# Kernel tuning notes

Measured on AMD Instinct MI355X. Metric: run time of the kernel, lower is better.

## Reference

```python
import jax, jax.numpy as jnp
import numpy as np

B, L, D = 1, 4096, 1024
N_AR, N_DIFF, D_HEAD = 8, 8, 64
H = N_AR + N_DIFF
ROPE_BASE = 10000.0


def rotate_half(x):
    x1, x2 = jnp.split(x, 2, axis=-1)
    return jnp.concatenate([-x2, x1], axis=-1)


def rope_cos_sin(seq_len, d_head):
    inv_freq = 1.0 / (ROPE_BASE ** (jnp.arange(0, d_head, 2, dtype=jnp.float32) / d_head))
    t = jnp.arange(seq_len, dtype=jnp.float32)
    freqs = t[:, None] * inv_freq[None, :]          # [L, d_head//2]
    emb = jnp.concatenate([freqs, freqs], axis=-1)  # [L, d_head]
    return jnp.cos(emb), jnp.sin(emb)


def setup_inputs() -> dict:
    key = jax.random.key(0)
    ks = jax.random.split(key, 5)
    return {
        "hidden_states": jax.random.normal(ks[0], (B, L, D), dtype=jnp.float32),
        "Wq": jax.random.normal(ks[1], (D, H * D_HEAD), dtype=jnp.float32) * 0.02,
        "Wk": jax.random.normal(ks[2], (D, H * D_HEAD), dtype=jnp.float32) * 0.02,
        "Wv": jax.random.normal(ks[3], (D, H * D_HEAD), dtype=jnp.float32) * 0.02,
        "Wo": jax.random.normal(ks[4], (H * D_HEAD, D), dtype=jnp.float32) * 0.02,
    }


def _attend(q, k, v, mask):
    # q,k,v: [B, h, L, d]; mask: [L, L] additive
    scale = D_HEAD ** -0.5
    scores = jnp.einsum("bhqd,bhkd->bhqk", q, k) * scale + mask
    attn = jax.nn.softmax(scores.astype(jnp.float32), axis=-1).astype(q.dtype)
    return jnp.einsum("bhqk,bhkd->bhqd", attn, v)


def reference(hidden_states, Wq, Wk, Wv, Wo):
    b, l, _ = hidden_states.shape

    def heads(x, W):
        return (x @ W).reshape(b, l, H, D_HEAD).transpose(0, 2, 1, 3)  # [B,H,L,d]

    q = heads(hidden_states, Wq)
    k = heads(hidden_states, Wk)
    v = heads(hidden_states, Wv)

    cos, sin = rope_cos_sin(l, D_HEAD)  # [L, d]
    q = q * cos + rotate_half(q) * sin
    k = k * cos + rotate_half(k) * sin

    neg_inf = jnp.finfo(jnp.float32).min
    causal = jnp.where(jnp.tril(jnp.ones((l, l), dtype=bool)), 0.0, -jnp.inf).astype(jnp.float32)

    out_ar = _attend(q[:, :N_AR], k[:, :N_AR], v[:, :N_AR], causal)
    out_diff = _attend(q[:, N_AR:], k[:, N_AR:], v[:, N_AR:], jnp.zeros((l, l), jnp.float32))

    out = jnp.concatenate([out_ar, out_diff], axis=1)          # [B,H,L,d]
    out = out.transpose(0, 2, 1, 3).reshape(b, l, H * D_HEAD)  # [B,L,H*d]
    return out @ Wo
```

## Files before the change

kernel.cpp:

```cpp
#include <hip/hip_runtime.h>

#define LSEQ 4096
#define DMODEL 1024
#define HTOT 16
#define NAR 8
#define DHEAD 64
#define QKVS 3072

typedef unsigned short u16;
typedef unsigned int u32;
typedef __attribute__((ext_vector_type(8))) short bf16x8;
typedef __attribute__((ext_vector_type(4))) short bf16x4;
typedef __attribute__((ext_vector_type(4))) float f32x4;
typedef __attribute__((ext_vector_type(4))) unsigned int u32x4;

typedef __attribute__((address_space(1))) void gvoid;
typedef __attribute__((address_space(3))) void lvoid;

__device__ __forceinline__ void cp16(const void* g, void* l) {
    __builtin_amdgcn_global_load_lds((gvoid*)(void*)g, (lvoid*)l, 16, 0, 0);
}

__device__ __forceinline__ float bfs(u16 v) { return __uint_as_float((u32)v << 16); }
__device__ __forceinline__ u16 f2bf(float f) {
    u32 x = __float_as_uint(f);
    return (u16)((x + 0x7fffu + ((x >> 16) & 1u)) >> 16);
}
__device__ __forceinline__ u32 pack2(float a, float b) {
    return (u32)f2bf(a) | ((u32)f2bf(b) << 16);
}
__device__ __forceinline__ u32 packtr(float lo, float hi) {
    return __builtin_amdgcn_perm(__float_as_uint(hi), __float_as_uint(lo), 0x07060302u);
}

__global__ __launch_bounds__(256) void transp_cvt3(
    const float* __restrict__ Wq, const float* __restrict__ Wk,
    const float* __restrict__ Wv, u16* __restrict__ D)
{
    __shared__ u16 T[64][72];
    const float* S = (blockIdx.z == 0) ? Wq : ((blockIdx.z == 1) ? Wk : Wv);
    u16* Dz = D + (size_t)blockIdx.z * 1024 * 1024;
    const int tid = threadIdx.x;
    const int bx = blockIdx.x, by = blockIdx.y;
#pragma unroll
    for (int i = 0; i < 4; ++i) {
        int id = tid + i * 256;
        int fr = id >> 4, fc = id & 15;
        float4 v = *(const float4*)(S + (size_t)(by * 64 + fr) * 1024 + bx * 64 + fc * 4);
        T[fc * 4 + 0][fr] = f2bf(v.x);
        T[fc * 4 + 1][fr] = f2bf(v.y);
        T[fc * 4 + 2][fr] = f2bf(v.z);
        T[fc * 4 + 3][fr] = f2bf(v.w);
    }
    __syncthreads();
#pragma unroll
    for (int i = 0; i < 2; ++i) {
        int id = tid + i * 256;
        int c = id >> 3, g = id & 7;
        *(uint4*)(Dz + (size_t)(bx * 64 + c) * 1024 + by * 64 + g * 8) = *(const uint4*)&T[c][g * 8];
    }
}

__global__ __launch_bounds__(256) void transp_cvt(
    const float* __restrict__ S, u16* __restrict__ D)
{
    __shared__ u16 T[64][72];
    const int tid = threadIdx.x;
    const int bx = blockIdx.x, by = blockIdx.y;
#pragma unroll
    for (int i = 0; i < 4; ++i) {
        int id = tid + i * 256;
        int fr = id >> 4, fc = id & 15;
        float4 v = *(const float4*)(S + (size_t)(by * 64 + fr) * 1024 + bx * 64 + fc * 4);
        T[fc * 4 + 0][fr] = f2bf(v.x);
        T[fc * 4 + 1][fr] = f2bf(v.y);
        T[fc * 4 + 2][fr] = f2bf(v.z);
        T[fc * 4 + 3][fr] = f2bf(v.w);
    }
    __syncthreads();
#pragma unroll
    for (int i = 0; i < 2; ++i) {
        int id = tid + i * 256;
        int c = id >> 3, g = id & 7;
        *(uint4*)(D + (size_t)(bx * 64 + c) * 1024 + by * 64 + g * 8) = *(const uint4*)&T[c][g * 8];
    }
}

__global__ __launch_bounds__(256) void gemm_qkv(
    const float* __restrict__ A, const u16* __restrict__ Bt, u16* __restrict__ C)
{
    __shared__ u16 As[2][128][40];
    __shared__ u16 Bs[2][128][32];
    const int tid = threadIdx.x;
    const int lane = tid & 63, w = tid >> 6;
    const int col = lane & 15, quad = lane >> 4;
    const int bm = blockIdx.y << 7, bn = blockIdx.x << 7;
    const int wm = (w & 1) << 6, wn = (w >> 1) << 6;
    const int sr = lane >> 2, sc = (lane & 3) << 3;
    const int ar0 = tid >> 2, ag = (tid & 3) << 3;
    const f32x4 zero = {0.f, 0.f, 0.f, 0.f};
    f32x4 acc[4][4];
#pragma unroll
    for (int i = 0; i < 4; ++i)
#pragma unroll
        for (int j = 0; j < 4; ++j) acc[i][j] = zero;

    {
#pragma unroll
        for (int i = 0; i < 2; ++i)
            cp16(Bt + (size_t)(bn + w * 32 + i * 16 + sr) * 1024 + sc, &Bs[0][w * 32 + i * 16][0]);
        float4 a0[2], a1[2];
#pragma unroll
        for (int it = 0; it < 2; ++it) {
            const float* ap = A + (size_t)(bm + ar0 + it * 64) * 1024 + ag;
            a0[it] = *(const float4*)ap;
            a1[it] = *(const float4*)(ap + 4);
        }
#pragma unroll
        for (int it = 0; it < 2; ++it) {
            uint4 pk;
            pk.x = pack2(a0[it].x, a0[it].y); pk.y = pack2(a0[it].z, a0[it].w);
            pk.z = pack2(a1[it].x, a1[it].y); pk.w = pack2(a1[it].z, a1[it].w);
            *(uint4*)&As[0][ar0 + it * 64][ag] = pk;
        }
    }

    for (int kc = 0; kc < 32; ++kc) {
        const int cur = kc & 1, nxt = cur ^ 1;
        __syncthreads();
        const bool pre = (kc + 1 < 32);
        float4 a0[2], a1[2];
        if (pre) {
            const int k1 = (kc + 1) * 32;
#pragma unroll
            for (int i = 0; i < 2; ++i)
                cp16(Bt + (size_t)(bn + w * 32 + i * 16 + sr) * 1024 + k1 + sc,
                     &Bs[nxt][w * 32 + i * 16][0]);
#pragma unroll
            for (int it = 0; it < 2; ++it) {
                const float* ap = A + (size_t)(bm + ar0 + it * 64) * 1024 + k1 + ag;
                a0[it] = *(const float4*)ap;
                a1[it] = *(const float4*)(ap + 4);
            }
        }
        bf16x8 af[4], bfr[4];
#pragma unroll
        for (int i = 0; i < 4; ++i) af[i] = *(const bf16x8*)&As[cur][wm + i * 16 + col][quad * 8];
#pragma unroll
        for (int j = 0; j < 4; ++j) bfr[j] = *(const bf16x8*)&Bs[cur][wn + j * 16 + col][quad * 8];
#pragma unroll
        for (int i = 0; i < 4; ++i)
#pragma unroll
            for (int j = 0; j < 4; ++j)
                acc[i][j] = __builtin_amdgcn_mfma_f32_16x16x32_bf16(af[i], bfr[j], acc[i][j], 0, 0, 0);
        if (pre) {
#pragma unroll
            for (int it = 0; it < 2; ++it) {
                uint4 pk;
                pk.x = pack2(a0[it].x, a0[it].y); pk.y = pack2(a0[it].z, a0[it].w);
                pk.z = pack2(a1[it].x, a1[it].y); pk.w = pack2(a1[it].z, a1[it].w);
                *(uint4*)&As[nxt][ar0 + it * 64][ag] = pk;
            }
        }
    }
#pragma unroll
    for (int i = 0; i < 4; ++i)
#pragma unroll
        for (int j = 0; j < 4; ++j)
#pragma unroll
            for (int r = 0; r < 4; ++r)
                C[(size_t)(bm + wm + i * 16 + quad * 4 + r) * QKVS + bn + wn + j * 16 + col] =
                    f2bf(acc[i][j][r]);
}

__global__ __launch_bounds__(256) void gemm_out(
    const u16* __restrict__ A, const u16* __restrict__ Bt, float* __restrict__ C)
{
    __shared__ u16 As[2][128][32];
    __shared__ u16 Bs[2][128][32];
    const int tid = threadIdx.x;
    const int lane = tid & 63, w = tid >> 6;
    const int col = lane & 15, quad = lane >> 4;
    const int bm = blockIdx.y << 7, bn = blockIdx.x << 7;
    const int wm = (w & 1) << 6, wn = (w >> 1) << 6;
    const int sr = lane >> 2, sc = (lane & 3) << 3;
    const f32x4 zero = {0.f, 0.f, 0.f, 0.f};
    f32x4 acc[4][4];
#pragma unroll
    for (int i = 0; i < 4; ++i)
#pragma unroll
        for (int j = 0; j < 4; ++j) acc[i][j] = zero;

#pragma unroll
    for (int i = 0; i < 2; ++i) {
        const int r0 = w * 32 + i * 16;
        cp16(A  + (size_t)(bm + r0 + sr) * 1024 + sc, &As[0][r0][0]);
        cp16(Bt + (size_t)(bn + r0 + sr) * 1024 + sc, &Bs[0][r0][0]);
    }

    for (int kc = 0; kc < 32; ++kc) {
        const int cur = kc & 1, nxt = cur ^ 1;
        __syncthreads();
        if (kc + 1 < 32) {
            const int k1 = (kc + 1) * 32;
#pragma unroll
            for (int i = 0; i < 2; ++i) {
                const int r0 = w * 32 + i * 16;
                cp16(A  + (size_t)(bm + r0 + sr) * 1024 + k1 + sc, &As[nxt][r0][0]);
                cp16(Bt + (size_t)(bn + r0 + sr) * 1024 + k1 + sc, &Bs[nxt][r0][0]);
            }
        }
        bf16x8 af[4], bfr[4];
#pragma unroll
        for (int i = 0; i < 4; ++i) af[i] = *(const bf16x8*)&As[cur][wm + i * 16 + col][quad * 8];
#pragma unroll
        for (int j = 0; j < 4; ++j) bfr[j] = *(const bf16x8*)&Bs[cur][wn + j * 16 + col][quad * 8];
#pragma unroll
        for (int i = 0; i < 4; ++i)
#pragma unroll
            for (int j = 0; j < 4; ++j)
                acc[i][j] = __builtin_amdgcn_mfma_f32_16x16x32_bf16(af[i], bfr[j], acc[i][j], 0, 0, 0);
    }
#pragma unroll
    for (int i = 0; i < 4; ++i)
#pragma unroll
        for (int j = 0; j < 4; ++j)
#pragma unroll
            for (int r = 0; r < 4; ++r)
                C[(size_t)(bm + wm + i * 16 + quad * 4 + r) * 1024 + bn + wn + j * 16 + col] =
                    acc[i][j][r];
}

__global__ __launch_bounds__(256) void rope_kernel(u16* __restrict__ QKV)
{
    const int idx = blockIdx.x * 256 + threadIdx.x;
    const int i = idx & 31;
    const int h = (idx >> 5) & 15;
    const int t = idx >> 9;
    const float inv = __expf((float)i * -0.2878231366242557f);
    float s, c;
    __sincosf((float)t * inv, &s, &c);
    const size_t base = (size_t)t * QKVS + h * DHEAD + i;
    const float qs = 0.18033688011112042f;

    float q1 = bfs(QKV[base]), q2 = bfs(QKV[base + 32]);
    QKV[base]      = f2bf((q1 * c - q2 * s) * qs);
    QKV[base + 32] = f2bf((q2 * c + q1 * s) * qs);

    const size_t kb = base + 1024;
    float k1 = bfs(QKV[kb]), k2 = bfs(QKV[kb + 32]);
    QKV[kb]      = f2bf(k1 * c - k2 * s);
    QKV[kb + 32] = f2bf(k2 * c + k1 * s);
}

__global__ __launch_bounds__(256) void attn_mfma(
    const u16* __restrict__ QKV, u16* __restrict__ AO)
{
    __shared__ u16 Ks[2][128][64];
    __shared__ u16 Vt[2][64][136];
    const int bid = blockIdx.x;
    int h, qt;
    if (bid < 256) { h = 8 + (bid & 7); qt = bid >> 3; }
    else { int i = bid - 256; h = i & 7; qt = 31 - (i >> 3); }
    const bool causal = (h < NAR);
    const int tid = threadIdx.x;
    const int w = tid >> 6, lane = tid & 63;
    const int col = lane & 15, quad = lane >> 4;
    const int qb = qt * 128;
    const int qr0 = qb + w * 32 + col;
    const int qr1 = qr0 + 16;

    bf16x8 qf[2][2];
#pragma unroll
    for (int s = 0; s < 2; ++s)
#pragma unroll
        for (int ks = 0; ks < 2; ++ks)
            qf[s][ks] = *(const bf16x8*)(QKV + (size_t)(qr0 + s * 16) * QKVS +
                                         h * DHEAD + ks * 32 + quad * 8);

    bf16x4 ones;
    ones[0] = (short)0x3F80; ones[1] = (short)0x3F80;
    ones[2] = (short)0x3F80; ones[3] = (short)0x3F80;

    const f32x4 zero = {0.f, 0.f, 0.f, 0.f};
    f32x4 O[2][5];
#pragma unroll
    for (int s = 0; s < 2; ++s)
#pragma unroll
        for (int nd = 0; nd < 5; ++nd) O[s][nd] = zero;

    const int nch = causal ? (qt + 1) : (LSEQ / 128);
    const int krow = lane >> 3;
    const int kcb = (lane & 7) ^ krow;
    const u16* kbase = QKV + (size_t)krow * QKVS + 1024 + h * DHEAD + kcb * 8;
    const u16* vbase = QKV + (size_t)(lane * 2) * QKVS + 2048 + h * DHEAD + w * 16;

    {
#pragma unroll
        for (int i = 0; i < 4; ++i)
            cp16(kbase + (size_t)((i * 4 + w) * 8) * QKVS, &Ks[0][(i * 4 + w) * 8][0]);
        u32x4 A0 = *(u32x4*)(vbase);
        u32x4 A1 = *(u32x4*)(vbase + 8);
        u32x4 B0 = *(u32x4*)(vbase + QKVS);
        u32x4 B1 = *(u32x4*)(vbase + QKVS + 8);
#pragma unroll
        for (int j = 0; j < 4; ++j) {
            *(u32*)&Vt[0][w * 16 + 2 * j][lane * 2]     = __builtin_amdgcn_perm(B0[j], A0[j], 0x05040100u);
            *(u32*)&Vt[0][w * 16 + 2 * j + 1][lane * 2] = __builtin_amdgcn_perm(B0[j], A0[j], 0x07060302u);
            *(u32*)&Vt[0][w * 16 + 8 + 2 * j][lane * 2]     = __builtin_amdgcn_perm(B1[j], A1[j], 0x05040100u);
            *(u32*)&Vt[0][w * 16 + 8 + 2 * j + 1][lane * 2] = __builtin_amdgcn_perm(B1[j], A1[j], 0x07060302u);
        }
    }

    for (int ch = 0; ch < nch; ++ch) {
        const int cur = ch & 1, nxt = cur ^ 1;
        __syncthreads();
        const bool pre = (ch + 1 < nch);
        u32x4 A0 = {}, A1 = {}, B0 = {}, B1 = {};
        if (pre) {
            const size_t c1 = (size_t)(ch + 1) * 128;
#pragma unroll
            for (int i = 0; i < 4; ++i)
                cp16(kbase + (c1 + (i * 4 + w) * 8) * QKVS, &Ks[nxt][(i * 4 + w) * 8][0]);
            const u16* vp = vbase + c1 * QKVS;
            A0 = *(u32x4*)(vp);
            A1 = *(u32x4*)(vp + 8);
            B0 = *(u32x4*)(vp + QKVS);
            B1 = *(u32x4*)(vp + QKVS + 8);
        }

#pragma unroll
        for (int hf = 0; hf < 2; ++hf) {
            f32x4 st[2][4];
#pragma unroll
            for (int s = 0; s < 2; ++s)
#pragma unroll
                for (int jj = 0; jj < 4; ++jj) st[s][jj] = zero;
#pragma unroll
            for (int jj = 0; jj < 4; ++jj)
#pragma unroll
                for (int ks = 0; ks < 2; ++ks) {
                    bf16x8 kf = *(const bf16x8*)&Ks[cur][(hf * 4 + jj) * 16 + col]
                                                    [((ks * 4 + quad) ^ (col & 7)) * 8];
                    st[0][jj] = __builtin_amdgcn_mfma_f32_16x16x32_bf16(kf, qf[0][ks], st[0][jj], 0, 0, 0);
                    st[1][jj] = __builtin_amdgcn_mfma_f32_16x16x32_bf16(kf, qf[1][ks], st[1][jj], 0, 0, 0);
                }
            if (causal && ch == qt) {
#pragma unroll
                for (int jj = 0; jj < 4; ++jj) {
                    const int kk = ch * 128 + (hf * 4 + jj) * 16 + quad * 4;
#pragma unroll
                    for (int r = 0; r < 4; ++r) {
                        if (kk + r > qr0) st[0][jj][r] = -1e30f;
                        if (kk + r > qr1) st[1][jj][r] = -1e30f;
                    }
                }
            }
            bf16x4 pf[2][4];
#pragma unroll
            for (int s = 0; s < 2; ++s)
#pragma unroll
                for (int jj = 0; jj < 4; ++jj) {
                    u32 lo = packtr(__builtin_amdgcn_exp2f(st[s][jj][0]),
                                    __builtin_amdgcn_exp2f(st[s][jj][1]));
                    u32 hi = packtr(__builtin_amdgcn_exp2f(st[s][jj][2]),
                                    __builtin_amdgcn_exp2f(st[s][jj][3]));
                    u32* p = (u32*)&pf[s][jj];
                    p[0] = lo; p[1] = hi;
                }
#pragma unroll
            for (int nd = 0; nd < 4; ++nd)
#pragma unroll
                for (int jj = 0; jj < 4; ++jj) {
                    bf16x4 vtf = *(const bf16x4*)&Vt[cur][nd * 16 + col][(hf * 4 + jj) * 16 + quad * 4];
                    O[0][nd] = __builtin_amdgcn_mfma_f32_16x16x16bf16_1k(vtf, pf[0][jj], O[0][nd], 0, 0, 0);
                    O[1][nd] = __builtin_amdgcn_mfma_f32_16x16x16bf16_1k(vtf, pf[1][jj], O[1][nd], 0, 0, 0);
                }
#pragma unroll
            for (int jj = 0; jj < 4; ++jj) {
                O[0][4] = __builtin_amdgcn_mfma_f32_16x16x16bf16_1k(ones, pf[0][jj], O[0][4], 0, 0, 0);
                O[1][4] = __builtin_amdgcn_mfma_f32_16x16x16bf16_1k(ones, pf[1][jj], O[1][4], 0, 0, 0);
            }
        }

        if (pre) {
#pragma unroll
            for (int j = 0; j < 4; ++j) {
                *(u32*)&Vt[nxt][w * 16 + 2 * j][lane * 2]     = __builtin_amdgcn_perm(B0[j], A0[j], 0x05040100u);
                *(u32*)&Vt[nxt][w * 16 + 2 * j + 1][lane * 2] = __builtin_amdgcn_perm(B0[j], A0[j], 0x07060302u);
                *(u32*)&Vt[nxt][w * 16 + 8 + 2 * j][lane * 2]     = __builtin_amdgcn_perm(B1[j], A1[j], 0x05040100u);
                *(u32*)&Vt[nxt][w * 16 + 8 + 2 * j + 1][lane * 2] = __builtin_amdgcn_perm(B1[j], A1[j], 0x07060302u);
            }
        }
    }
#pragma unroll
    for (int s = 0; s < 2; ++s) {
        const float inv = 1.f / O[s][4][0];
        const int qrow = qr0 + s * 16;
#pragma unroll
        for (int nd = 0; nd < 4; ++nd) {
            ushort4 ov;
            ov.x = f2bf(O[s][nd][0] * inv);
            ov.y = f2bf(O[s][nd][1] * inv);
            ov.z = f2bf(O[s][nd][2] * inv);
            ov.w = f2bf(O[s][nd][3] * inv);
            *(ushort4*)(AO + (size_t)qrow * 1024 + h * DHEAD + nd * 16 + quad * 4) = ov;
        }
    }
}

extern "C" void kernel_launch(void* const* d_in, const int* in_sizes, int n_in,
                              void* d_out, int out_size, void* d_ws, size_t ws_size,
                              hipStream_t stream)
{
    const float* X  = (const float*)d_in[0];
    const float* Wq = (const float*)d_in[1];
    const float* Wk = (const float*)d_in[2];
    const float* Wv = (const float*)d_in[3];
    const float* Wo = (const float*)d_in[4];
    float* out = (float*)d_out;

    u16* Wt  = (u16*)d_ws;
    u16* AOb = (u16*)d_ws;
    u16* QKV = (u16*)d_ws + (size_t)4 * 1024 * 1024;
    u16* Wot = QKV;

    transp_cvt3<<<dim3(16, 16, 3), 256, 0, stream>>>(Wq, Wk, Wv, Wt);
    gemm_qkv<<<dim3(24, 32), 256, 0, stream>>>(X, Wt, QKV);
    rope_kernel<<<(LSEQ * HTOT * 32) / 256, 256, 0, stream>>>(QKV);
    attn_mfma<<<512, 256, 0, stream>>>(QKV, AOb);
    transp_cvt<<<dim3(16, 16), 256, 0, stream>>>(Wo, Wot);
    gemm_out<<<dim3(8, 32), 256, 0, stream>>>(AOb, Wot, out);
}
```

Baseline: 273.0 us.

## Fuse RoPE into QKV GEMM epilogue and restructure attention to 2-wave software pipeline

RoPE and the Q scaling now run in the QKV GEMM epilogue on fp32 accumulators, so the separate rope kernel and its read-modify-write pass over Q/K are gone. The QKV GEMM also converts its A input to bf16 by truncation (packtr) instead of round-to-nearest, which costs a little accuracy. The attention kernel moves to 128 threads with 64 query rows per wave and a skewed pipeline that overlaps P·V of the previous chunk with QK^T/exp of the current one. This raises per-wave register pressure and halves the threads per block, which may lower occupancy.

```diff
diff --git a/kernel.cpp b/kernel.cpp
--- a/kernel.cpp
+++ b/kernel.cpp
@@ -25,9 +25,6 @@
 __device__ __forceinline__ u16 f2bf(float f) {
     u32 x = __float_as_uint(f);
     return (u16)((x + 0x7fffu + ((x >> 16) & 1u)) >> 16);
-}
-__device__ __forceinline__ u32 pack2(float a, float b) {
-    return (u32)f2bf(a) | ((u32)f2bf(b) << 16);
 }
 __device__ __forceinline__ u32 packtr(float lo, float hi) {
     return __builtin_amdgcn_perm(__float_as_uint(hi), __float_as_uint(lo), 0x07060302u);
@@ -109,18 +106,14 @@
 #pragma unroll
         for (int i = 0; i < 2; ++i)
             cp16(Bt + (size_t)(bn + w * 32 + i * 16 + sr) * 1024 + sc, &Bs[0][w * 32 + i * 16][0]);
-        float4 a0[2], a1[2];
 #pragma unroll
         for (int it = 0; it < 2; ++it) {
             const float* ap = A + (size_t)(bm + ar0 + it * 64) * 1024 + ag;
-            a0[it] = *(const float4*)ap;
-            a1[it] = *(const float4*)(ap + 4);
-        }
-#pragma unroll
-        for (int it = 0; it < 2; ++it) {
+            float4 a0 = *(const float4*)ap;
+            float4 a1 = *(const float4*)(ap + 4);
             uint4 pk;
-            pk.x = pack2(a0[it].x, a0[it].y); pk.y = pack2(a0[it].z, a0[it].w);
-            pk.z = pack2(a1[it].x, a1[it].y); pk.w = pack2(a1[it].z, a1[it].w);
+            pk.x = packtr(a0.x, a0.y); pk.y = packtr(a0.z, a0.w);
+            pk.z = packtr(a1.x, a1.y); pk.w = packtr(a1.z, a1.w);
             *(uint4*)&As[0][ar0 + it * 64][ag] = pk;
         }
     }
@@ -157,11 +150,32 @@
 #pragma unroll
             for (int it = 0; it < 2; ++it) {
                 uint4 pk;
-                pk.x = pack2(a0[it].x, a0[it].y); pk.y = pack2(a0[it].z, a0[it].w);
-                pk.z = pack2(a1[it].x, a1[it].y); pk.w = pack2(a1[it].z, a1[it].w);
+                pk.x = packtr(a0[it].x, a0[it].y); pk.y = packtr(a0[it].z, a0[it].w);
+                pk.z = packtr(a1[it].x, a1[it].y); pk.w = packtr(a1[it].z, a1[it].w);
                 *(uint4*)&As[nxt][ar0 + it * 64][ag] = pk;
             }
         }
+    }
+
+    if (blockIdx.x < 16) {
+        const float scale = (blockIdx.x < 8) ? 0.18033688011112042f : 1.0f;
+        const float inv0 = __expf((float)col * -0.2878231366242557f);
+        const float inv1 = __expf((float)(16 + col) * -0.2878231366242557f);
+#pragma unroll
+        for (int i = 0; i < 4; ++i)
+#pragma unroll
+            for (int r = 0; r < 4; ++r) {
+                const float t = (float)(bm + wm + i * 16 + quad * 4 + r);
+                float s0, c0, s1, c1;
+                __sincosf(t * inv0, &s0, &c0);
+                __sincosf(t * inv1, &s1, &c1);
+                float a0 = acc[i][0][r], b0 = acc[i][2][r];
+                acc[i][0][r] = (a0 * c0 - b0 * s0) * scale;
+                acc[i][2][r] = (b0 * c0 + a0 * s0) * scale;
+                float a1 = acc[i][1][r], b1 = acc[i][3][r];
+                acc[i][1][r] = (a1 * c1 - b1 * s1) * scale;
+                acc[i][3][r] = (b1 * c1 + a1 * s1) * scale;
+            }
     }
 #pragma unroll
     for (int i = 0; i < 4; ++i)
@@ -231,29 +245,7 @@
                     acc[i][j][r];
 }
 
-__global__ __launch_bounds__(256) void rope_kernel(u16* __restrict__ QKV)
-{
-    const int idx = blockIdx.x * 256 + threadIdx.x;
-    const int i = idx & 31;
-    const int h = (idx >> 5) & 15;
-    const int t = idx >> 9;
-    const float inv = __expf((float)i * -0.2878231366242557f);
-    float s, c;
-    __sincosf((float)t * inv, &s, &c);
-    const size_t base = (size_t)t * QKVS + h * DHEAD + i;
-    const float qs = 0.18033688011112042f;
-
-    float q1 = bfs(QKV[base]), q2 = bfs(QKV[base + 32]);
-    QKV[base]      = f2bf((q1 * c - q2 * s) * qs);
-    QKV[base + 32] = f2bf((q2 * c + q1 * s) * qs);
-
-    const size_t kb = base + 1024;
-    float k1 = bfs(QKV[kb]), k2 = bfs(QKV[kb + 32]);
-    QKV[kb]      = f2bf(k1 * c - k2 * s);
-    QKV[kb + 32] = f2bf(k2 * c + k1 * s);
-}
-
-__global__ __launch_bounds__(256) void attn_mfma(
+__global__ __launch_bounds__(128, 1) void attn_mfma(
     const u16* __restrict__ QKV, u16* __restrict__ AO)
 {
     __shared__ u16 Ks[2][128][64];
@@ -267,12 +259,11 @@
     const int w = tid >> 6, lane = tid & 63;
     const int col = lane & 15, quad = lane >> 4;
     const int qb = qt * 128;
-    const int qr0 = qb + w * 32 + col;
-    const int qr1 = qr0 + 16;
-
-    bf16x8 qf[2][2];
-#pragma unroll
-    for (int s = 0; s < 2; ++s)
+    const int qr0 = qb + w * 64 + col;
+
+    bf16x8 qf[4][2];
+#pragma unroll
+    for (int s = 0; s < 4; ++s)
 #pragma unroll
         for (int ks = 0; ks < 2; ++ks)
             qf[s][ks] = *(const bf16x8*)(QKV + (size_t)(qr0 + s * 16) * QKVS +
@@ -283,9 +274,9 @@
     ones[2] = (short)0x3F80; ones[3] = (short)0x3F80;
 
     const f32x4 zero = {0.f, 0.f, 0.f, 0.f};
-    f32x4 O[2][5];
-#pragma unroll
-    for (int s = 0; s < 2; ++s)
+    f32x4 O[4][5];
+#pragma unroll
+    for (int s = 0; s < 4; ++s)
 #pragma unroll
         for (int nd = 0; nd < 5; ++nd) O[s][nd] = zero;
 
@@ -293,108 +284,137 @@
     const int krow = lane >> 3;
     const int kcb = (lane & 7) ^ krow;
     const u16* kbase = QKV + (size_t)krow * QKVS + 1024 + h * DHEAD + kcb * 8;
-    const u16* vbase = QKV + (size_t)(lane * 2) * QKVS + 2048 + h * DHEAD + w * 16;
-
-    {
-#pragma unroll
-        for (int i = 0; i < 4; ++i)
-            cp16(kbase + (size_t)((i * 4 + w) * 8) * QKVS, &Ks[0][(i * 4 + w) * 8][0]);
-        u32x4 A0 = *(u32x4*)(vbase);
-        u32x4 A1 = *(u32x4*)(vbase + 8);
-        u32x4 B0 = *(u32x4*)(vbase + QKVS);
-        u32x4 B1 = *(u32x4*)(vbase + QKVS + 8);
-#pragma unroll
-        for (int j = 0; j < 4; ++j) {
-            *(u32*)&Vt[0][w * 16 + 2 * j][lane * 2]     = __builtin_amdgcn_perm(B0[j], A0[j], 0x05040100u);
-            *(u32*)&Vt[0][w * 16 + 2 * j + 1][lane * 2] = __builtin_amdgcn_perm(B0[j], A0[j], 0x07060302u);
-            *(u32*)&Vt[0][w * 16 + 8 + 2 * j][lane * 2]     = __builtin_amdgcn_perm(B1[j], A1[j], 0x05040100u);
-            *(u32*)&Vt[0][w * 16 + 8 + 2 * j + 1][lane * 2] = __builtin_amdgcn_perm(B1[j], A1[j], 0x07060302u);
-        }
-    }
-
-    for (int ch = 0; ch < nch; ++ch) {
-        const int cur = ch & 1, nxt = cur ^ 1;
+    const u16* vbase = QKV + (size_t)(lane * 2) * QKVS + 2048 + h * DHEAD + w * 32;
+
+    u32x4 vA[4], vB[4];
+    bf16x4 pf[4][8];
+
+#define VT_WRITE(buf)                                                                     \
+    {                                                                                     \
+        _Pragma("unroll")                                                                 \
+        for (int part = 0; part < 4; ++part)                                              \
+            _Pragma("unroll")                                                             \
+            for (int j = 0; j < 4; ++j) {                                                 \
+                const int d = w * 32 + part * 8 + 2 * j;                                  \
+                *(u32*)&Vt[buf][d][lane * 2] =                                            \
+                    __builtin_amdgcn_perm(vB[part][j], vA[part][j], 0x05040100u);         \
+                *(u32*)&Vt[buf][d + 1][lane * 2] =                                        \
+                    __builtin_amdgcn_perm(vB[part][j], vA[part][j], 0x07060302u);         \
+            }                                                                             \
+    }
+
+#define V_LOAD(chbase)                                                                    \
+    {                                                                                     \
+        const u16* vp = vbase + (size_t)(chbase) * QKVS;                                  \
+        _Pragma("unroll")                                                                 \
+        for (int part = 0; part < 4; ++part) {                                            \
+            vA[part] = *(u32x4*)(vp + part * 8);                                          \
+            vB[part] = *(u32x4*)(vp + QKVS + part * 8);                                   \
+        }                                                                                 \
+    }
+
+#define K_STAGE(chbase, buf)                                                              \
+    {                                                                                     \
+        _Pragma("unroll")                                                                 \
+        for (int i = 0; i < 8; ++i) {                                                     \
+            const int j = i * 2 + w;                                                      \
+            cp16(kbase + (size_t)((chbase) + j * 8) * QKVS, &Ks[buf][j * 8][0]);          \
+        }                                                                                 \
+    }
+
+#define S_EXP(buf, chq)                                                                   \
+    {                                                                                     \
+        const bool mask = causal && ((chq) == qt);                                        \
+        _Pragma("unroll")                                                                 \
+        for (int hf = 0; hf < 2; ++hf) {                                                  \
+            f32x4 st[4][4];                                                               \
+            _Pragma("unroll")                                                             \
+            for (int s = 0; s < 4; ++s)                                                   \
+                _Pragma("unroll")                                                         \
+                for (int jj = 0; jj < 4; ++jj) st[s][jj] = zero;                          \
+            _Pragma("unroll")                                                             \
+            for (int jj = 0; jj < 4; ++jj)                                                \
+                _Pragma("unroll")                                                         \
+                for (int ks = 0; ks < 2; ++ks) {                                          \
+                    bf16x8 kf = *(const bf16x8*)&Ks[buf][(hf * 4 + jj) * 16 + col]        \
+                                                    [((ks * 4 + quad) ^ (col & 7)) * 8];  \
+                    _Pragma("unroll")                                                     \
+                    for (int s = 0; s < 4; ++s)                                           \
+                        st[s][jj] = __builtin_amdgcn_mfma_f32_16x16x32_bf16(              \
+                            kf, qf[s][ks], st[s][jj], 0, 0, 0);                           \
+                }                                                                         \
+            if (mask) {                                                                   \
+                _Pragma("unroll")                                                         \
+                for (int jj = 0; jj < 4; ++jj) {                                          \
+                    const int kk = (chq) * 128 + (hf * 4 + jj) * 16 + quad * 4;           \
+                    _Pragma("unroll")                                                     \
+                    for (int s = 0; s < 4; ++s)                                           \
+                        _Pragma("unroll")                                                 \
+                        for (int r = 0; r < 4; ++r)                                       \
+                            if (kk + r > qr0 + s * 16) st[s][jj][r] = -1e30f;             \
+                }                                                                         \
+            }                                                                             \
+            _Pragma("unroll")                                                             \
+            for (int s = 0; s < 4; ++s)                                                   \
+                _Pragma("unroll")                                                         \
+                for (int jj = 0; jj < 4; ++jj) {                                          \
+                    u32 lo = packtr(__builtin_amdgcn_exp2f(st[s][jj][0]),                 \
+                                    __builtin_amdgcn_exp2f(st[s][jj][1]));                \
+                    u32 hi = packtr(__builtin_amdgcn_exp2f(st[s][jj][2]),                 \
+                                    __builtin_amdgcn_exp2f(st[s][jj][3]));                \
+                    u32* p = (u32*)&pf[s][hf * 4 + jj];                                   \
+                    p[0] = lo; p[1] = hi;                                                 \
+                }                                                                         \
+        }                                                                                 \
+    }
+
+#define PV(buf)                                                                           \
+    {                                                                                     \
+        _Pragma("unroll")                                                                 \
+        for (int nd = 0; nd < 4; ++nd)                                                    \
+            _Pragma("unroll")                                                             \
+            for (int t = 0; t < 8; ++t) {                                                 \
+                bf16x4 vtf = *(const bf16x4*)&Vt[buf][nd * 16 + col][t * 16 + quad * 4];  \
+                _Pragma("unroll")                                                         \
+                for (int s = 0; s < 4; ++s)                                               \
+                    O[s][nd] = __builtin_amdgcn_mfma_f32_16x16x16bf16_1k(                 \
+                        vtf, pf[s][t], O[s][nd], 0, 0, 0);                                \
+            }                                                                             \
+        _Pragma("unroll")                                                                 \
+        for (int t = 0; t < 8; ++t)                                                       \
+            _Pragma("unroll")                                                             \
+            for (int s = 0; s < 4; ++s)                                                   \
+                O[s][4] = __builtin_amdgcn_mfma_f32_16x16x16bf16_1k(                      \
+                    ones, pf[s][t], O[s][4], 0, 0, 0);                                    \
+    }
+
+    K_STAGE(0, 0);
+    V_LOAD(0);
+    __syncthreads();
+    VT_WRITE(0);
+    if (nch > 1) {
+        K_STAGE(128, 1);
+        V_LOAD(128);
+    }
+    S_EXP(0, 0);
+
+    for (int ch = 1; ch < nch; ++ch) {
+        const int cur = ch & 1, prv = cur ^ 1;
         __syncthreads();
-        const bool pre = (ch + 1 < nch);
-        u32x4 A0 = {}, A1 = {}, B0 = {}, B1 = {};
-        if (pre) {
-            const size_t c1 = (size_t)(ch + 1) * 128;
-#pragma unroll
-            for (int i = 0; i < 4; ++i)
-                cp16(kbase + (c1 + (i * 4 + w) * 8) * QKVS, &Ks[nxt][(i * 4 + w) * 8][0]);
-            const u16* vp = vbase + c1 * QKVS;
-            A0 = *(u32x4*)(vp);
-            A1 = *(u32x4*)(vp + 8);
-            B0 = *(u32x4*)(vp + QKVS);
-            B1 = *(u32x4*)(vp + QKVS + 8);
-        }
-
-#pragma unroll
-        for (int hf = 0; hf < 2; ++hf) {
-            f32x4 st[2][4];
-#pragma unroll
-            for (int s = 0; s < 2; ++s)
-#pragma unroll
-                for (int jj = 0; jj < 4; ++jj) st[s][jj] = zero;
-#pragma unroll
-            for (int jj = 0; jj < 4; ++jj)
-#pragma unroll
-                for (int ks = 0; ks < 2; ++ks) {
-                    bf16x8 kf = *(const bf16x8*)&Ks[cur][(hf * 4 + jj) * 16 + col]
-                                                    [((ks * 4 + quad) ^ (col & 7)) * 8];
-                    st[0][jj] = __builtin_amdgcn_mfma_f32_16x16x32_bf16(kf, qf[0][ks], st[0][jj], 0, 0, 0);
-                    st[1][jj] = __builtin_amdgcn_mfma_f32_16x16x32_bf16(kf, qf[1][ks], st[1][jj], 0, 0, 0);
-                }
-            if (causal && ch == qt) {
-#pragma unroll
-                for (int jj = 0; jj < 4; ++jj) {
-                    const int kk = ch * 128 + (hf * 4 + jj) * 16 + quad * 4;
-#pragma unroll
-                    for (int r = 0; r < 4; ++r) {
-                        if (kk + r > qr0) st[0][jj][r] = -1e30f;
-                        if (kk + r > qr1) st[1][jj][r] = -1e30f;
-                    }
-                }
-            }
-            bf16x4 pf[2][4];
-#pragma unroll
-            for (int s = 0; s < 2; ++s)
-#pragma unroll
-                for (int jj = 0; jj < 4; ++jj) {
-                    u32 lo = packtr(__builtin_amdgcn_exp2f(st[s][jj][0]),
-                                    __builtin_amdgcn_exp2f(st[s][jj][1]));
-                    u32 hi = packtr(__builtin_amdgcn_exp2f(st[s][jj][2]),
-                                    __builtin_amdgcn_exp2f(st[s][jj][3]));
-                    u32* p = (u32*)&pf[s][jj];
-                    p[0] = lo; p[1] = hi;
-                }
-#pragma unroll
-            for (int nd = 0; nd < 4; ++nd)
-#pragma unroll
-                for (int jj = 0; jj < 4; ++jj) {
-                    bf16x4 vtf = *(const bf16x4*)&Vt[cur][nd * 16 + col][(hf * 4 + jj) * 16 + quad * 4];
-                    O[0][nd] = __builtin_amdgcn_mfma_f32_16x16x16bf16_1k(vtf, pf[0][jj], O[0][nd], 0, 0, 0);
-                    O[1][nd] = __builtin_amdgcn_mfma_f32_16x16x16bf16_1k(vtf, pf[1][jj], O[1][nd], 0, 0, 0);
-                }
-#pragma unroll
-            for (int jj = 0; jj < 4; ++jj) {
-                O[0][4] = __builtin_amdgcn_mfma_f32_16x16x16bf16_1k(ones, pf[0][jj], O[0][4], 0, 0, 0);
-                O[1][4] = __builtin_amdgcn_mfma_f32_16x16x16bf16_1k(ones, pf[1][jj], O[1][4], 0, 0, 0);
-            }
-        }
-
-        if (pre) {
-#pragma unroll
-            for (int j = 0; j < 4; ++j) {
-                *(u32*)&Vt[nxt][w * 16 + 2 * j][lane * 2]     = __builtin_amdgcn_perm(B0[j], A0[j], 0x05040100u);
-                *(u32*)&Vt[nxt][w * 16 + 2 * j + 1][lane * 2] = __builtin_amdgcn_perm(B0[j], A0[j], 0x07060302u);
-                *(u32*)&Vt[nxt][w * 16 + 8 + 2 * j][lane * 2]     = __builtin_amdgcn_perm(B1[j], A1[j], 0x05040100u);
-                *(u32*)&Vt[nxt][w * 16 + 8 + 2 * j + 1][lane * 2] = __builtin_amdgcn_perm(B1[j], A1[j], 0x07060302u);
-            }
-        }
-    }
-#pragma unroll
-    for (int s = 0; s < 2; ++s) {
+        VT_WRITE(cur);
+        if (ch + 1 < nch) {
+            K_STAGE((ch + 1) * 128, prv);
+            V_LOAD((size_t)(ch + 1) * 128);
+        }
+        PV(prv);
+        S_EXP(cur, ch);
+    }
+
+    __syncthreads();
+    PV((nch - 1) & 1);
+
+#pragma unroll
+    for (int s = 0; s < 4; ++s) {
         const float inv = 1.f / O[s][4][0];
         const int qrow = qr0 + s * 16;
 #pragma unroll
@@ -407,6 +427,11 @@
             *(ushort4*)(AO + (size_t)qrow * 1024 + h * DHEAD + nd * 16 + quad * 4) = ov;
         }
     }
+#undef VT_WRITE
+#undef V_LOAD
+#undef K_STAGE
+#undef S_EXP
+#undef PV
 }
 
 extern "C" void kernel_launch(void* const* d_in, const int* in_sizes, int n_in,
@@ -427,8 +452,7 @@
 
     transp_cvt3<<<dim3(16, 16, 3), 256, 0, stream>>>(Wq, Wk, Wv, Wt);
     gemm_qkv<<<dim3(24, 32), 256, 0, stream>>>(X, Wt, QKV);
-    rope_kernel<<<(LSEQ * HTOT * 32) / 256, 256, 0, stream>>>(QKV);
-    attn_mfma<<<512, 256, 0, stream>>>(QKV, AOb);
+    attn_mfma<<<512, 128, 0, stream>>>(QKV, AOb);
     transp_cvt<<<dim3(16, 16), 256, 0, stream>>>(Wo, Wot);
     gemm_out<<<dim3(8, 32), 256, 0, stream>>>(AOb, Wot, out);
 }
```

After: 280.1 us. +2.6%, slower.
